# Optimization experiments

Measured on AMD Instinct MI355X. Metric: run time of the kernel, lower is better.

The kernel has to match this reference:

```python
import jax, jax.numpy as jnp
import numpy as np

D_MODEL = 512      # hidden_dim
D_INNER = 1024     # 2 * hidden_dim (Mamba expand=2)
D_STATE = 16       # SSM state size N
DT_RANK = 32       # hidden_dim // 16
NBLK = 4           # num_blocks
KCONV = 4          # depthwise conv kernel
NHEAD = 4
NUM_LANES = 6
LANE_DIM = 128


def _rms(x, w, eps=1e-5):
    return x * jax.lax.rsqrt(jnp.mean(x * x, axis=-1, keepdims=True) + eps) * w


def _selective_scan(u, delta, A, Bm, Cm, Dv):
    # u, delta: [B,L,d]; A: [d,N]; Bm, Cm: [B,L,N]; Dv: [d]
    dA = jnp.exp(delta[..., None] * A)                 # [B,L,d,N]
    dBu = (delta * u)[..., None] * Bm[:, :, None, :]   # [B,L,d,N]

    def step(h, xs):
        dA_t, dBu_t = xs
        h = dA_t * h + dBu_t
        return h, h

    h0 = jnp.zeros(dA.shape[:1] + dA.shape[2:], dA.dtype)  # [B,d,N]
    _, hs = jax.lax.scan(step, h0, (jnp.swapaxes(dA, 0, 1), jnp.swapaxes(dBu, 0, 1)))
    y = jnp.einsum('lbdn,bln->bld', hs, Cm)            # [B,L,d]
    return y + u * Dv


def _mamba(lane_features, lane_in_W, lane_in_b, norm_w, in_proj_W, conv_w, conv_b,
           x_proj_W, dt_proj_W, dt_proj_b, A_log, D_skip, out_proj_W, final_norm_w):
    x = lane_features @ lane_in_W + lane_in_b          # [B,L,D_MODEL]
    for i in range(NBLK):
        h = _rms(x, norm_w[i])
        xz = h @ in_proj_W[i]                          # [B,L,2*D_INNER]
        xc, z = jnp.split(xz, 2, axis=-1)
        xt = jnp.swapaxes(xc, 1, 2)                    # [B,d,L]
        conv = jax.lax.conv_general_dilated(
            xt, conv_w[i][:, None, :], (1,), [(KCONV - 1, 0)],
            feature_group_count=D_INNER,
            dimension_numbers=('NCH', 'OIH', 'NCH')) + conv_b[i][:, None]
        xc = jax.nn.silu(jnp.swapaxes(conv, 1, 2))     # causal depthwise conv + SiLU
        dbl = xc @ x_proj_W[i]
        dt = dbl[..., :DT_RANK]
        Bm = dbl[..., DT_RANK:DT_RANK + D_STATE]
        Cm = dbl[..., DT_RANK + D_STATE:]
        delta = jax.nn.softplus(dt @ dt_proj_W[i] + dt_proj_b[i])
        y = _selective_scan(xc, delta, -jnp.exp(A_log[i]), Bm, Cm, D_skip[i])
        x = x + (y * jax.nn.silu(z)) @ out_proj_W[i]
    return _rms(x, final_norm_w)


def _mha(q_in, kv_in, Wq, bq, Wk, bk, Wv, bv, Wo, bo):
    B, Lq, _ = q_in.shape
    Lk = kv_in.shape[1]
    dh = D_MODEL // NHEAD
    q = (q_in @ Wq + bq).reshape(B, Lq, NHEAD, dh).transpose(0, 2, 1, 3)
    k = (kv_in @ Wk + bk).reshape(B, Lk, NHEAD, dh).transpose(0, 2, 1, 3)
    v = (kv_in @ Wv + bv).reshape(B, Lk, NHEAD, dh).transpose(0, 2, 1, 3)
    attn = jax.nn.softmax(jnp.einsum('bhqd,bhkd->bhqk', q, k) / np.sqrt(dh).astype(np.float32), axis=-1)
    o = jnp.einsum('bhqk,bhkd->bhqd', attn, v).transpose(0, 2, 1, 3).reshape(B, Lq, D_MODEL)
    return o @ Wo + bo


def setup_inputs() -> dict:
    key = jax.random.key(0)
    ks = iter(jax.random.split(key, 40))
    def n(shape, s=0.02):
        return jax.random.normal(next(ks), shape, jnp.float32) * s
    inp = {}
    inp['agent_features'] = jax.random.normal(next(ks), (8, 256, D_MODEL), jnp.float32)
    inp['lane_features'] = jax.random.normal(next(ks), (8, 512, LANE_DIM), jnp.float32)
    inp['lane_in_W'] = n((LANE_DIM, D_MODEL))
    inp['lane_in_b'] = jnp.zeros((D_MODEL,), jnp.float32)
    inp['norm_w'] = jnp.ones((NBLK, D_MODEL), jnp.float32)
    inp['in_proj_W'] = n((NBLK, D_MODEL, 2 * D_INNER))
    inp['conv_w'] = n((NBLK, D_INNER, KCONV), 0.2)
    inp['conv_b'] = jnp.zeros((NBLK, D_INNER), jnp.float32)
    inp['x_proj_W'] = n((NBLK, D_INNER, DT_RANK + 2 * D_STATE))
    inp['dt_proj_W'] = n((NBLK, DT_RANK, D_INNER), 0.1)
    inp['dt_proj_b'] = n((NBLK, D_INNER), 0.1)
    inp['A_log'] = jnp.tile(jnp.log(jnp.arange(1, D_STATE + 1, dtype=jnp.float32)), (NBLK, D_INNER, 1))
    inp['D_skip'] = jnp.ones((NBLK, D_INNER), jnp.float32)
    inp['out_proj_W'] = n((NBLK, D_INNER, D_MODEL))
    inp['final_norm_w'] = jnp.ones((D_MODEL,), jnp.float32)
    for name in ['Wq', 'Wk', 'Wv', 'Wo']:
        inp[name] = n((D_MODEL, D_MODEL))
    for name in ['bq', 'bk', 'bv', 'bo']:
        inp[name] = jnp.zeros((D_MODEL,), jnp.float32)
    inp['lin_in_W'] = n((D_MODEL, D_MODEL))
    inp['lin_in_b'] = jnp.zeros((D_MODEL,), jnp.float32)
    inp['lin_out_W'] = n((D_MODEL, NUM_LANES))
    inp['lin_out_b'] = jnp.zeros((NUM_LANES,), jnp.float32)
    return inp


def reference(agent_features, lane_features, lane_in_W, lane_in_b, norm_w, in_proj_W,
              conv_w, conv_b, x_proj_W, dt_proj_W, dt_proj_b, A_log, D_skip, out_proj_W,
              final_norm_w, Wq, Wk, Wv, Wo, bq, bk, bv, bo,
              lin_in_W, lin_in_b, lin_out_W, lin_out_b):
    enhanced = _mamba(lane_features, lane_in_W, lane_in_b, norm_w, in_proj_W, conv_w,
                      conv_b, x_proj_W, dt_proj_W, dt_proj_b, A_log, D_skip,
                      out_proj_W, final_norm_w)
    attn_out = _mha(enhanced, agent_features, Wq, bq, Wk, bk, Wv, bv, Wo, bo)
    probs = (attn_out @ lin_in_W + lin_in_b) @ lin_out_W + lin_out_b
    preds = jnp.argmax(probs, axis=-1)
    return probs, preds
```

## Files before the change

### kernel.cpp

```cpp
#include <hip/hip_runtime.h>
#include <math.h>

#define BATCH 8
#define LSEQ 512
#define LAGENT 256
#define DMODEL 512
#define DINNER 1024
#define DSTATE 16
#define DTRANK 32
#define NHEAD 4
#define DHEAD 128
#define NLANES 6

typedef __attribute__((ext_vector_type(8))) short bf16x8;
typedef __attribute__((ext_vector_type(4))) float f32x4;

__device__ __forceinline__ void split3(float x, short& h, short& m, short& l)
{
    unsigned hb = __float_as_uint(x) & 0xFFFF0000u;
    h = (short)(hb >> 16);
    float r1 = x - __uint_as_float(hb);
    unsigned mb = __float_as_uint(r1) & 0xFFFF0000u;
    m = (short)(mb >> 16);
    float r2 = r1 - __uint_as_float(mb);
    l = (short)(__float_as_uint(r2) >> 16);
}

template<int BM, int BN, int WM, int WN>
__global__ __launch_bounds__(256)
void gemm6(const float* __restrict__ A, int lda,
           const float* __restrict__ W,
           const float* __restrict__ bias,
           float* __restrict__ C, int ldc,
           int M, int N, int K, int act, int addC)
{
    constexpr int MT = BM / WM / 16;
    constexpr int NT = BN / WN / 16;
    constexpr int ASL = BM / 16;
    constexpr int BSL = BN / 16;
    __shared__ short Asl[3][ASL * 520];
    __shared__ short Bsl[3][BSL * 520];

    const int tid = threadIdx.x;
    const int w = tid >> 6, lane = tid & 63;
    const int lrow = lane & 15, quad = lane >> 4;
    const int aslab0 = (w % WM) * MT;
    const int bslab0 = (w / WM) * NT;
    const int m0 = blockIdx.y * BM, n0 = blockIdx.x * BN;

    f32x4 acc[MT][NT] = {};

    for (int k0 = 0; k0 < K; k0 += 32) {
        __syncthreads();
#pragma unroll
        for (int i = 0; i < BM / 32; ++i) {
            int v = tid + 256 * i;
            int row = v >> 3;
            int kq = (v & 7) * 4;
            float4 val = *(const float4*)&A[(size_t)(m0 + row) * lda + k0 + kq];
            int off = (row >> 4) * 520 + (((kq >> 3) << 4) + (row & 15)) * 8 + (kq & 7);
            short h[4], mm_[4], l[4];
            split3(val.x, h[0], mm_[0], l[0]);
            split3(val.y, h[1], mm_[1], l[1]);
            split3(val.z, h[2], mm_[2], l[2]);
            split3(val.w, h[3], mm_[3], l[3]);
            *(short4*)&Asl[0][off] = make_short4(h[0], h[1], h[2], h[3]);
            *(short4*)&Asl[1][off] = make_short4(mm_[0], mm_[1], mm_[2], mm_[3]);
            *(short4*)&Asl[2][off] = make_short4(l[0], l[1], l[2], l[3]);
        }
        constexpr int NPQS = (BN == 128) ? 5 : 4;
#pragma unroll
        for (int i = 0; i < BN / 64; ++i) {
            int v = tid + 256 * i;
            int kp = v >> NPQS;
            int nc = (v & ((1 << NPQS) - 1)) * 4;
            int k1 = kp * 2;
            float4 r0 = *(const float4*)&W[(size_t)(k0 + k1) * N + n0 + nc];
            float4 r1 = *(const float4*)&W[(size_t)(k0 + k1 + 1) * N + n0 + nc];
            const float e0[4] = {r0.x, r0.y, r0.z, r0.w};
            const float e1[4] = {r1.x, r1.y, r1.z, r1.w};
#pragma unroll
            for (int e = 0; e < 4; ++e) {
                int n = nc + e;
                int off = (n >> 4) * 520 + (((k1 >> 3) << 4) + (n & 15)) * 8 + (k1 & 7);
                short h0, m0_, l0, h1, m1_, l1;
                split3(e0[e], h0, m0_, l0);
                split3(e1[e], h1, m1_, l1);
                *(short2*)&Bsl[0][off] = make_short2(h0, h1);
                *(short2*)&Bsl[1][off] = make_short2(m0_, m1_);
                *(short2*)&Bsl[2][off] = make_short2(l0, l1);
            }
        }
        __syncthreads();

        bf16x8 af[3][MT];
#pragma unroll
        for (int p = 0; p < 3; ++p)
#pragma unroll
            for (int i = 0; i < MT; ++i)
                af[p][i] = *(const bf16x8*)&Asl[p][(aslab0 + i) * 520 + lane * 8];

#pragma unroll
        for (int pb = 0; pb < 3; ++pb) {
            bf16x8 bfr[NT];
#pragma unroll
            for (int j = 0; j < NT; ++j)
                bfr[j] = *(const bf16x8*)&Bsl[pb][(bslab0 + j) * 520 + lane * 8];
            const int npa = (pb == 0) ? 3 : (pb == 1 ? 2 : 1);
#pragma unroll
            for (int pa = 0; pa < 3; ++pa) {
                if (pa >= npa) break;
#pragma unroll
                for (int i = 0; i < MT; ++i)
#pragma unroll
                    for (int j = 0; j < NT; ++j)
                        acc[i][j] = __builtin_amdgcn_mfma_f32_16x16x32_bf16(
                            af[pa][i], bfr[j], acc[i][j], 0, 0, 0);
            }
        }
    }

#pragma unroll
    for (int i = 0; i < MT; ++i) {
        int mbase = m0 + (aslab0 + i) * 16 + quad * 4;
#pragma unroll
        for (int j = 0; j < NT; ++j) {
            int n = n0 + (bslab0 + j) * 16 + lrow;
            float bv = bias ? bias[n] : 0.f;
#pragma unroll
            for (int r = 0; r < 4; ++r) {
                size_t off = (size_t)(mbase + r) * ldc + n;
                float v = acc[i][j][r] + bv;
                if (act == 1) v = (v > 20.f) ? v : log1pf(__expf(v));
                if (addC) v += C[off];
                C[off] = v;
            }
        }
    }
}

template<int BM, int BN, int WM, int WN>
__global__ __launch_bounds__(256)
void gemm6p(const unsigned short* __restrict__ Ap0,
            const unsigned short* __restrict__ Ap1,
            const unsigned short* __restrict__ Ap2, int lda,
            const float* __restrict__ W,
            const float* __restrict__ bias,
            float* __restrict__ C, int ldc,
            int M, int N, int K, int act, int addC)
{
    constexpr int MT = BM / WM / 16;
    constexpr int NT = BN / WN / 16;
    constexpr int ASL = BM / 16;
    constexpr int BSL = BN / 16;
    __shared__ short Asl[3][ASL * 520];
    __shared__ short Bsl[3][BSL * 520];

    const int tid = threadIdx.x;
    const int w = tid >> 6, lane = tid & 63;
    const int lrow = lane & 15, quad = lane >> 4;
    const int aslab0 = (w % WM) * MT;
    const int bslab0 = (w / WM) * NT;
    const int m0 = blockIdx.y * BM, n0 = blockIdx.x * BN;

    f32x4 acc[MT][NT] = {};

    for (int k0 = 0; k0 < K; k0 += 32) {
        __syncthreads();
#pragma unroll
        for (int i = 0; i < BM / 32; ++i) {
            int v = tid + 256 * i;
            int row = v >> 3;
            int kq = (v & 7) * 4;
            size_t g = (size_t)(m0 + row) * lda + k0 + kq;
            int off = (row >> 4) * 520 + (((kq >> 3) << 4) + (row & 15)) * 8 + (kq & 7);
            *(short4*)&Asl[0][off] = *(const short4*)&Ap0[g];
            *(short4*)&Asl[1][off] = *(const short4*)&Ap1[g];
            *(short4*)&Asl[2][off] = *(const short4*)&Ap2[g];
        }
        constexpr int NPQS = (BN == 128) ? 5 : 4;
#pragma unroll
        for (int i = 0; i < BN / 64; ++i) {
            int v = tid + 256 * i;
            int kp = v >> NPQS;
            int nc = (v & ((1 << NPQS) - 1)) * 4;
            int k1 = kp * 2;
            float4 r0 = *(const float4*)&W[(size_t)(k0 + k1) * N + n0 + nc];
            float4 r1 = *(const float4*)&W[(size_t)(k0 + k1 + 1) * N + n0 + nc];
            const float e0[4] = {r0.x, r0.y, r0.z, r0.w};
            const float e1[4] = {r1.x, r1.y, r1.z, r1.w};
#pragma unroll
            for (int e = 0; e < 4; ++e) {
                int n = nc + e;
                int off = (n >> 4) * 520 + (((k1 >> 3) << 4) + (n & 15)) * 8 + (k1 & 7);
                short h0, m0_, l0, h1, m1_, l1;
                split3(e0[e], h0, m0_, l0);
                split3(e1[e], h1, m1_, l1);
                *(short2*)&Bsl[0][off] = make_short2(h0, h1);
                *(short2*)&Bsl[1][off] = make_short2(m0_, m1_);
                *(short2*)&Bsl[2][off] = make_short2(l0, l1);
            }
        }
        __syncthreads();

        bf16x8 af[3][MT];
#pragma unroll
        for (int p = 0; p < 3; ++p)
#pragma unroll
            for (int i = 0; i < MT; ++i)
                af[p][i] = *(const bf16x8*)&Asl[p][(aslab0 + i) * 520 + lane * 8];

#pragma unroll
        for (int pb = 0; pb < 3; ++pb) {
            bf16x8 bfr[NT];
#pragma unroll
            for (int j = 0; j < NT; ++j)
                bfr[j] = *(const bf16x8*)&Bsl[pb][(bslab0 + j) * 520 + lane * 8];
            const int npa = (pb == 0) ? 3 : (pb == 1 ? 2 : 1);
#pragma unroll
            for (int pa = 0; pa < 3; ++pa) {
                if (pa >= npa) break;
#pragma unroll
                for (int i = 0; i < MT; ++i)
#pragma unroll
                    for (int j = 0; j < NT; ++j)
                        acc[i][j] = __builtin_amdgcn_mfma_f32_16x16x32_bf16(
                            af[pa][i], bfr[j], acc[i][j], 0, 0, 0);
            }
        }
    }

#pragma unroll
    for (int i = 0; i < MT; ++i) {
        int mbase = m0 + (aslab0 + i) * 16 + quad * 4;
#pragma unroll
        for (int j = 0; j < NT; ++j) {
            int n = n0 + (bslab0 + j) * 16 + lrow;
            float bv = bias ? bias[n] : 0.f;
#pragma unroll
            for (int r = 0; r < 4; ++r) {
                size_t off = (size_t)(mbase + r) * ldc + n;
                float v = acc[i][j][r] + bv;
                if (act == 1) v = (v > 20.f) ? v : log1pf(__expf(v));
                if (addC) v += C[off];
                C[off] = v;
            }
        }
    }
}

__global__ __launch_bounds__(256)
void gemm6sk(const float* __restrict__ A, int lda,
             const float* __restrict__ W, int N,
             float* __restrict__ P, int M, int KC)
{
    constexpr int BM = 64, BN = 64, WM = 2, WN = 2;
    constexpr int MT = BM / WM / 16, NT = BN / WN / 16;
    __shared__ short Asl[3][4 * 520];
    __shared__ short Bsl[3][4 * 520];

    const int tid = threadIdx.x;
    const int w = tid >> 6, lane = tid & 63;
    const int lrow = lane & 15, quad = lane >> 4;
    const int aslab0 = (w % WM) * MT;
    const int bslab0 = (w / WM) * NT;
    const int m0 = blockIdx.y * BM, n0 = blockIdx.x * BN;
    const int kbeg = blockIdx.z * KC;

    f32x4 acc[MT][NT] = {};

    for (int k0 = kbeg; k0 < kbeg + KC; k0 += 32) {
        __syncthreads();
#pragma unroll
        for (int i = 0; i < BM / 32; ++i) {
            int v = tid + 256 * i;
            int row = v >> 3;
            int kq = (v & 7) * 4;
            float4 val = *(const float4*)&A[(size_t)(m0 + row) * lda + k0 + kq];
            int off = (row >> 4) * 520 + (((kq >> 3) << 4) + (row & 15)) * 8 + (kq & 7);
            short h[4], mm_[4], l[4];
            split3(val.x, h[0], mm_[0], l[0]);
            split3(val.y, h[1], mm_[1], l[1]);
            split3(val.z, h[2], mm_[2], l[2]);
            split3(val.w, h[3], mm_[3], l[3]);
            *(short4*)&Asl[0][off] = make_short4(h[0], h[1], h[2], h[3]);
            *(short4*)&Asl[1][off] = make_short4(mm_[0], mm_[1], mm_[2], mm_[3]);
            *(short4*)&Asl[2][off] = make_short4(l[0], l[1], l[2], l[3]);
        }
        {
            int v = tid;
            int kp = v >> 4;
            int nc = (v & 15) * 4;
            int k1 = kp * 2;
            float4 r0 = *(const float4*)&W[(size_t)(k0 + k1) * N + n0 + nc];
            float4 r1 = *(const float4*)&W[(size_t)(k0 + k1 + 1) * N + n0 + nc];
            const float e0[4] = {r0.x, r0.y, r0.z, r0.w};
            const float e1[4] = {r1.x, r1.y, r1.z, r1.w};
#pragma unroll
            for (int e = 0; e < 4; ++e) {
                int n = nc + e;
                int off = (n >> 4) * 520 + (((k1 >> 3) << 4) + (n & 15)) * 8 + (k1 & 7);
                short h0, m0_, l0, h1, m1_, l1;
                split3(e0[e], h0, m0_, l0);
                split3(e1[e], h1, m1_, l1);
                *(short2*)&Bsl[0][off] = make_short2(h0, h1);
                *(short2*)&Bsl[1][off] = make_short2(m0_, m1_);
                *(short2*)&Bsl[2][off] = make_short2(l0, l1);
            }
        }
        __syncthreads();

        bf16x8 af[3][MT];
#pragma unroll
        for (int p = 0; p < 3; ++p)
#pragma unroll
            for (int i = 0; i < MT; ++i)
                af[p][i] = *(const bf16x8*)&Asl[p][(aslab0 + i) * 520 + lane * 8];

#pragma unroll
        for (int pb = 0; pb < 3; ++pb) {
            bf16x8 bfr[NT];
#pragma unroll
            for (int j = 0; j < NT; ++j)
                bfr[j] = *(const bf16x8*)&Bsl[pb][(bslab0 + j) * 520 + lane * 8];
            const int npa = (pb == 0) ? 3 : (pb == 1 ? 2 : 1);
#pragma unroll
            for (int pa = 0; pa < 3; ++pa) {
                if (pa >= npa) break;
#pragma unroll
                for (int i = 0; i < MT; ++i)
#pragma unroll
                    for (int j = 0; j < NT; ++j)
                        acc[i][j] = __builtin_amdgcn_mfma_f32_16x16x32_bf16(
                            af[pa][i], bfr[j], acc[i][j], 0, 0, 0);
            }
        }
    }

    float* Pz = P + (size_t)blockIdx.z * M * N;
#pragma unroll
    for (int i = 0; i < MT; ++i) {
        int mbase = m0 + (aslab0 + i) * 16 + quad * 4;
#pragma unroll
        for (int j = 0; j < NT; ++j) {
            int n = n0 + (bslab0 + j) * 16 + lrow;
#pragma unroll
            for (int r = 0; r < 4; ++r)
                Pz[(size_t)(mbase + r) * N + n] = acc[i][j][r];
        }
    }
}

__global__ __launch_bounds__(256)
void xred_k(const float* __restrict__ P, float* __restrict__ D)
{
    int i = blockIdx.x * 256 + threadIdx.x;
    const float4* p = (const float4*)P;
    float4 a = p[i];
#pragma unroll
    for (int z = 1; z < 8; ++z) {
        float4 b = p[(size_t)z * 65536 + i];
        a.x += b.x; a.y += b.y; a.z += b.z; a.w += b.w;
    }
    ((float4*)D)[i] = a;
}

__global__ __launch_bounds__(256)
void rmsnorm3_k(const float* __restrict__ X, const float* __restrict__ w,
                unsigned short* __restrict__ P0, unsigned short* __restrict__ P1,
                unsigned short* __restrict__ P2)
{
    int wid = threadIdx.x >> 6, lane = threadIdx.x & 63;
    int row = blockIdx.x * 4 + wid;
    const float* xr = X + (size_t)row * DMODEL;
    float v[8];
    float ss = 0.f;
#pragma unroll
    for (int j = 0; j < 8; ++j) { v[j] = xr[lane + 64 * j]; ss = fmaf(v[j], v[j], ss); }
#pragma unroll
    for (int off = 32; off >= 1; off >>= 1) ss += __shfl_xor(ss, off);
    float scale = rsqrtf(ss * (1.f / 512.f) + 1e-5f);
#pragma unroll
    for (int j = 0; j < 8; ++j) {
        int col = lane + 64 * j;
        float val = v[j] * scale * w[col];
        short hh, mm, ll;
        split3(val, hh, mm, ll);
        size_t o = (size_t)row * DMODEL + col;
        P0[o] = (unsigned short)hh;
        P1[o] = (unsigned short)mm;
        P2[o] = (unsigned short)ll;
    }
}

__global__ __launch_bounds__(256)
void conv_silu_k(const float* __restrict__ XZ, const float* __restrict__ cw,
                 const float* __restrict__ cb, float* __restrict__ XC)
{
    int idx = blockIdx.x * 256 + threadIdx.x;
    int d4 = (idx & 255) * 4;
    int t = (idx >> 8) & 511;
    int b = idx >> 17;
    float4 wv[4];
#pragma unroll
    for (int e = 0; e < 4; ++e) wv[e] = *(const float4*)&cw[(d4 + e) * 4];
    float4 bv = *(const float4*)&cb[d4];
    float s[4] = {bv.x, bv.y, bv.z, bv.w};
#pragma unroll
    for (int k = 0; k < 4; ++k) {
        int tt = t + k - 3;
        if (tt >= 0) {
            float4 x = *(const float4*)&XZ[((size_t)(b * 512 + tt)) * 2048 + d4];
            const float xe[4] = {x.x, x.y, x.z, x.w};
            const float we[4] = {wv[0][k], wv[1][k], wv[2][k], wv[3][k]};
#pragma unroll
            for (int e = 0; e < 4; ++e) s[e] = fmaf(we[e], xe[e], s[e]);
        }
    }
    float4 o;
    o.x = s[0] / (1.f + __expf(-s[0]));
    o.y = s[1] / (1.f + __expf(-s[1]));
    o.z = s[2] / (1.f + __expf(-s[2]));
    o.w = s[3] / (1.f + __expf(-s[3]));
    *(float4*)&XC[((size_t)(b * 512 + t)) * 1024 + d4] = o;
}

__global__ __launch_bounds__(128)
void scan1_k(const float* __restrict__ DELTA, const float* __restrict__ XC,
             const float* __restrict__ DBL, const float* __restrict__ A_log,
             const float* __restrict__ Dsk, float* __restrict__ Y,
             float* __restrict__ SC, float* __restrict__ DS)
{
    __shared__ float BC[64][32];
    const int tid = threadIdx.x;
    const int d = blockIdx.x * 128 + tid;
    const int chunk = blockIdx.y;
    const int b = blockIdx.z;
    const int t0 = chunk * 64;

#pragma unroll
    for (int i = 0; i < 16; ++i) {
        int idx = tid + 128 * i;
        int t = idx >> 5, j = idx & 31;
        BC[t][j] = DBL[(size_t)(b * 512 + t0 + t) * 64 + 32 + j];
    }
    float Ac[16];
#pragma unroll
    for (int n = 0; n < 16; ++n) Ac[n] = -__expf(A_log[d * 16 + n]);
    float Dv = Dsk[d];
    __syncthreads();

    const float* dp = DELTA + ((size_t)(b * 512 + t0)) * 1024 + d;
    const float* up = XC    + ((size_t)(b * 512 + t0)) * 1024 + d;
    float* yp       = Y     + ((size_t)(b * 512 + t0)) * 1024 + d;

    float h[16];
#pragma unroll
    for (int n = 0; n < 16; ++n) h[n] = 0.f;
    float dsum = 0.f;

#pragma unroll 2
    for (int t = 0; t < 64; ++t) {
        float delta = dp[t * 1024];
        float u = up[t * 1024];
        dsum += delta;
        float du = delta * u;
        float y = 0.f;
#pragma unroll
        for (int n = 0; n < 16; ++n) {
            h[n] = fmaf(__expf(delta * Ac[n]), h[n], du * BC[t][n]);
            y = fmaf(h[n], BC[t][16 + n], y);
        }
        yp[t * 1024] = fmaf(u, Dv, y);
    }

    float* sc = SC + ((size_t)((b * 8 + chunk) * 1024 + d)) * 16;
#pragma unroll
    for (int n = 0; n < 16; ++n) sc[n] = h[n];
    DS[(size_t)(b * 8 + chunk) * 1024 + d] = dsum;
}

__global__ __launch_bounds__(256)
void scan2_k(const float* __restrict__ A_log, float* __restrict__ SC,
             const float* __restrict__ DS)
{
    int gid = blockIdx.x * 256 + threadIdx.x;
    int n = gid & 15;
    int d = (gid >> 4) & 1023;
    int b = gid >> 14;
    float Ac = -__expf(A_log[d * 16 + n]);
    float carry = 0.f;
#pragma unroll
    for (int c = 0; c < 8; ++c) {
        size_t off = ((size_t)((b * 8 + c) * 1024 + d)) * 16 + n;
        float s = SC[off];
        SC[off] = carry;
        carry = fmaf(__expf(Ac * DS[(size_t)(b * 8 + c) * 1024 + d]), carry, s);
    }
}

__global__ __launch_bounds__(128)
void scan3_k(const float* __restrict__ DELTA, const float* __restrict__ DBL,
             const float* __restrict__ A_log, const float* __restrict__ H0,
             const float* __restrict__ XZ, float* __restrict__ Y)
{
    __shared__ float Cs[64][16];
    const int tid = threadIdx.x;
    const int d = blockIdx.x * 128 + tid;
    const int chunk = blockIdx.y;
    const int b = blockIdx.z;
    const int t0 = chunk * 64;

#pragma unroll
    for (int i = 0; i < 8; ++i) {
        int idx = tid + 128 * i;
        int t = idx >> 4, j = idx & 15;
        Cs[t][j] = DBL[(size_t)(b * 512 + t0 + t) * 64 + 48 + j];
    }
    float Ac[16], h0[16];
#pragma unroll
    for (int n = 0; n < 16; ++n) Ac[n] = -__expf(A_log[d * 16 + n]);
    const float* h0p = H0 + ((size_t)((b * 8 + chunk) * 1024 + d)) * 16;
#pragma unroll
    for (int n = 0; n < 16; ++n) h0[n] = h0p[n];
    __syncthreads();

    const float* dp = DELTA + ((size_t)(b * 512 + t0)) * 1024 + d;
    const float* zp = XZ    + ((size_t)(b * 512 + t0)) * 2048 + 1024 + d;
    float* yp       = Y     + ((size_t)(b * 512 + t0)) * 1024 + d;

    float cum = 0.f;
    if (chunk == 0) {
#pragma unroll 2
        for (int t = 0; t < 64; ++t) {
            float z = zp[t * 2048];
            yp[t * 1024] *= z / (1.f + __expf(-z));
        }
    } else {
#pragma unroll 2
        for (int t = 0; t < 64; ++t) {
            float delta = dp[t * 1024];
            cum += delta;
            float p = 0.f;
#pragma unroll
            for (int n = 0; n < 16; ++n)
                p = fmaf(h0[n] * __expf(Ac[n] * cum), Cs[t][n], p);
            float z = zp[t * 2048];
            float yv = yp[t * 1024] + p;
            yp[t * 1024] = yv * (z / (1.f + __expf(-z)));
        }
    }
}

__global__ __launch_bounds__(256, 1)
void attn_mfma(const float* __restrict__ Qm, const float* __restrict__ Km,
               const float* __restrict__ Vm, float* __restrict__ CTX)
{
    __shared__ short KVs[3][16 * 520];
    __shared__ float Ps[4][16 * 260];
    const int tid = threadIdx.x;
    const int w = tid >> 6, lane = tid & 63;
    const int lrow = lane & 15, quad = lane >> 4;
    const int b = blockIdx.z, h = blockIdx.y;
    const int qw = blockIdx.x * 64 + w * 16;

    bf16x8 qf[3][4];
    {
        const float* qp = Qm + ((size_t)(b * 512 + qw + lrow)) * 512 + h * 128 + quad * 8;
#pragma unroll
        for (int kb = 0; kb < 4; ++kb) {
            float4 v0 = *(const float4*)(qp + kb * 32);
            float4 v1 = *(const float4*)(qp + kb * 32 + 4);
            const float e[8] = {v0.x, v0.y, v0.z, v0.w, v1.x, v1.y, v1.z, v1.w};
#pragma unroll
            for (int j = 0; j < 8; ++j) {
                short hh, mm, ll;
                split3(e[j], hh, mm, ll);
                qf[0][kb][j] = hh; qf[1][kb][j] = mm; qf[2][kb][j] = ll;
            }
        }
    }

    const int sdd = (tid & 31) * 4;
    const int skvb = tid >> 5;
    f32x4 sa[4][4] = {};

    float4 kpre[8];
#pragma unroll
    for (int i = 0; i < 8; ++i)
        kpre[i] = *(const float4*)&Km[((size_t)(b * 256 + skvb + 8 * i)) * 512 + h * 128 + sdd];

    for (int c = 0; c < 4; ++c) {
        if (c) __syncthreads();
        {
            const int kb = sdd >> 5, qd = (sdd >> 3) & 3, jd = sdd & 7;
#pragma unroll
            for (int i = 0; i < 8; ++i) {
                int kv = skvb + 8 * i;
                int off = ((kv >> 4) * 4 + kb) * 520 + ((kv & 15) + 16 * qd) * 8 + jd;
                short h0,m0,l0,h1,m1,l1,h2,m2,l2,h3,m3,l3;
                split3(kpre[i].x,h0,m0,l0); split3(kpre[i].y,h1,m1,l1);
                split3(kpre[i].z,h2,m2,l2); split3(kpre[i].w,h3,m3,l3);
                *(short4*)&KVs[0][off] = make_short4(h0,h1,h2,h3);
                *(short4*)&KVs[1][off] = make_short4(m0,m1,m2,m3);
                *(short4*)&KVs[2][off] = make_short4(l0,l1,l2,l3);
            }
        }
        if (c < 3) {
#pragma unroll
            for (int i = 0; i < 8; ++i)
                kpre[i] = *(const float4*)&Km[((size_t)(b * 256 + (c + 1) * 64 + skvb + 8 * i)) * 512 + h * 128 + sdd];
        }
        __syncthreads();
#pragma unroll
        for (int s = 0; s < 4; ++s) {
#pragma unroll
            for (int kb = 0; kb < 4; ++kb) {
                bf16x8 kf[3];
#pragma unroll
                for (int p = 0; p < 3; ++p)
                    kf[p] = *(const bf16x8*)&KVs[p][(s * 4 + kb) * 520 + lane * 8];
                sa[c][s] = __builtin_amdgcn_mfma_f32_16x16x32_bf16(qf[0][kb], kf[0], sa[c][s], 0, 0, 0);
                sa[c][s] = __builtin_amdgcn_mfma_f32_16x16x32_bf16(qf[0][kb], kf[1], sa[c][s], 0, 0, 0);
                sa[c][s] = __builtin_amdgcn_mfma_f32_16x16x32_bf16(qf[1][kb], kf[0], sa[c][s], 0, 0, 0);
                sa[c][s] = __builtin_amdgcn_mfma_f32_16x16x32_bf16(qf[0][kb], kf[2], sa[c][s], 0, 0, 0);
                sa[c][s] = __builtin_amdgcn_mfma_f32_16x16x32_bf16(qf[1][kb], kf[1], sa[c][s], 0, 0, 0);
                sa[c][s] = __builtin_amdgcn_mfma_f32_16x16x32_bf16(qf[2][kb], kf[0], sa[c][s], 0, 0, 0);
            }
        }
    }

    const float scale = 0.08838834764831845f;
    float mx[4] = {-1e30f, -1e30f, -1e30f, -1e30f};
#pragma unroll
    for (int c = 0; c < 4; ++c)
#pragma unroll
        for (int s = 0; s < 4; ++s)
#pragma unroll
            for (int r = 0; r < 4; ++r) {
                sa[c][s][r] *= scale;
                mx[r] = fmaxf(mx[r], sa[c][s][r]);
            }
#pragma unroll
    for (int r = 0; r < 4; ++r) {
        mx[r] = fmaxf(mx[r], __shfl_xor(mx[r], 1));
        mx[r] = fmaxf(mx[r], __shfl_xor(mx[r], 2));
        mx[r] = fmaxf(mx[r], __shfl_xor(mx[r], 4));
        mx[r] = fmaxf(mx[r], __shfl_xor(mx[r], 8));
    }
    float sum[4] = {0.f, 0.f, 0.f, 0.f};
#pragma unroll
    for (int c = 0; c < 4; ++c)
#pragma unroll
        for (int s = 0; s < 4; ++s)
#pragma unroll
            for (int r = 0; r < 4; ++r) {
                float e = __expf(sa[c][s][r] - mx[r]);
                sa[c][s][r] = e;
                sum[r] += e;
            }
#pragma unroll
    for (int r = 0; r < 4; ++r) {
        sum[r] += __shfl_xor(sum[r], 1);
        sum[r] += __shfl_xor(sum[r], 2);
        sum[r] += __shfl_xor(sum[r], 4);
        sum[r] += __shfl_xor(sum[r], 8);
        sum[r] = 1.f / sum[r];
    }
    {
        float* ps = &Ps[w][0];
#pragma unroll
        for (int c = 0; c < 4; ++c)
#pragma unroll
            for (int s = 0; s < 4; ++s)
#pragma unroll
                for (int r = 0; r < 4; ++r)
                    ps[(quad * 4 + r) * 260 + c * 64 + s * 16 + lrow] = sa[c][s][r] * sum[r];
    }

    const int vdd4 = (tid & 31) * 4;
    const int vkvg = tid >> 5;
    f32x4 oa[8] = {};
    float4 vpre[8];
#pragma unroll
    for (int i = 0; i < 2; ++i) {
        int kv0 = (vkvg + 8 * i) * 4;
#pragma unroll
        for (int rr = 0; rr < 4; ++rr)
            vpre[i * 4 + rr] = *(const float4*)&Vm[((size_t)(b * 256 + kv0 + rr)) * 512 + h * 128 + vdd4];
    }

    for (int c = 0; c < 4; ++c) {
        __syncthreads();
        {
#pragma unroll
            for (int i = 0; i < 2; ++i) {
                int kv0 = (vkvg + 8 * i) * 4;
                int kb2 = kv0 >> 5, qk = (kv0 >> 3) & 3, jb = kv0 & 7;
                const float4 r0 = vpre[i * 4 + 0], r1 = vpre[i * 4 + 1];
                const float4 r2 = vpre[i * 4 + 2], r3 = vpre[i * 4 + 3];
                const float ve[4][4] = {{r0.x, r1.x, r2.x, r3.x},
                                        {r0.y, r1.y, r2.y, r3.y},
                                        {r0.z, r1.z, r2.z, r3.z},
                                        {r0.w, r1.w, r2.w, r3.w}};
#pragma unroll
                for (int e = 0; e < 4; ++e) {
                    int dd = vdd4 + e;
                    int off = ((dd >> 4) * 2 + kb2) * 520 + ((dd & 15) + 16 * qk) * 8 + jb;
                    short h0,m0,l0,h1,m1,l1,h2,m2,l2,h3,m3,l3;
                    split3(ve[e][0],h0,m0,l0); split3(ve[e][1],h1,m1,l1);
                    split3(ve[e][2],h2,m2,l2); split3(ve[e][3],h3,m3,l3);
                    *(short4*)&KVs[0][off] = make_short4(h0,h1,h2,h3);
                    *(short4*)&KVs[1][off] = make_short4(m0,m1,m2,m3);
                    *(short4*)&KVs[2][off] = make_short4(l0,l1,l2,l3);
                }
            }
        }
        if (c < 3) {
#pragma unroll
            for (int i = 0; i < 2; ++i) {
                int kv0 = (vkvg + 8 * i) * 4;
#pragma unroll
                for (int rr = 0; rr < 4; ++rr)
                    vpre[i * 4 + rr] = *(const float4*)&Vm[((size_t)(b * 256 + (c + 1) * 64 + kv0 + rr)) * 512 + h * 128 + vdd4];
            }
        }
        __syncthreads();
#pragma unroll
        for (int kb2 = 0; kb2 < 2; ++kb2) {
            const float* pp = &Ps[w][lrow * 260 + c * 64 + kb2 * 32 + quad * 8];
            float4 a0 = *(const float4*)pp;
            float4 a1 = *(const float4*)(pp + 4);
            const float e[8] = {a0.x, a0.y, a0.z, a0.w, a1.x, a1.y, a1.z, a1.w};
            bf16x8 af[3];
#pragma unroll
            for (int j = 0; j < 8; ++j) {
                short hh, mm, ll;
                split3(e[j], hh, mm, ll);
                af[0][j] = hh; af[1][j] = mm; af[2][j] = ll;
            }
#pragma unroll
            for (int s = 0; s < 8; ++s) {
                bf16x8 vf[3];
#pragma unroll
                for (int p = 0; p < 3; ++p)
                    vf[p] = *(const bf16x8*)&KVs[p][(s * 2 + kb2) * 520 + lane * 8];
                oa[s] = __builtin_amdgcn_mfma_f32_16x16x32_bf16(af[0], vf[0], oa[s], 0, 0, 0);
                oa[s] = __builtin_amdgcn_mfma_f32_16x16x32_bf16(af[0], vf[1], oa[s], 0, 0, 0);
                oa[s] = __builtin_amdgcn_mfma_f32_16x16x32_bf16(af[1], vf[0], oa[s], 0, 0, 0);
                oa[s] = __builtin_amdgcn_mfma_f32_16x16x32_bf16(af[0], vf[2], oa[s], 0, 0, 0);
                oa[s] = __builtin_amdgcn_mfma_f32_16x16x32_bf16(af[1], vf[1], oa[s], 0, 0, 0);
                oa[s] = __builtin_amdgcn_mfma_f32_16x16x32_bf16(af[2], vf[0], oa[s], 0, 0, 0);
            }
        }
    }

#pragma unroll
    for (int s = 0; s < 8; ++s)
#pragma unroll
        for (int r = 0; r < 4; ++r)
            CTX[((size_t)(b * 512 + qw + quad * 4 + r)) * 512 + h * 128 + s * 16 + lrow] = oa[s][r];
}

__global__ __launch_bounds__(256)
void head_k(const float* __restrict__ T2, const float* __restrict__ Wout,
            const float* __restrict__ bout, float* __restrict__ out)
{
    int wid = threadIdx.x >> 6, lane = threadIdx.x & 63;
    int row = blockIdx.x * 4 + wid;
    float acc[6] = {0.f, 0.f, 0.f, 0.f, 0.f, 0.f};
    const float* tr = T2 + (size_t)row * 512;
#pragma unroll
    for (int j = 0; j < 8; ++j) {
        int k = lane + 64 * j;
        float t = tr[k];
#pragma unroll
        for (int c = 0; c < 6; ++c) acc[c] = fmaf(t, Wout[k * 6 + c], acc[c]);
    }
#pragma unroll
    for (int c = 0; c < 6; ++c) {
#pragma unroll
        for (int off = 32; off >= 1; off >>= 1) acc[c] += __shfl_xor(acc[c], off);
    }
    if (lane == 0) {
        float best = -1e30f;
        int bi = 0;
#pragma unroll
        for (int c = 0; c < 6; ++c) {
            float v = acc[c] + bout[c];
            out[(size_t)row * 6 + c] = v;
            if (v > best) { best = v; bi = c; }
        }
        out[(size_t)4096 * 6 + row] = (float)bi;
    }
}

extern "C" void kernel_launch(void* const* d_in, const int* in_sizes, int n_in,
                              void* d_out, int out_size, void* d_ws, size_t ws_size,
                              hipStream_t stream)
{
    (void)in_sizes; (void)n_in; (void)out_size; (void)ws_size;
    const float* agent      = (const float*)d_in[0];
    const float* lane       = (const float*)d_in[1];
    const float* lane_in_W  = (const float*)d_in[2];
    const float* lane_in_b  = (const float*)d_in[3];
    const float* norm_w     = (const float*)d_in[4];
    const float* in_proj_W  = (const float*)d_in[5];
    const float* conv_w     = (const float*)d_in[6];
    const float* conv_b     = (const float*)d_in[7];
    const float* x_proj_W   = (const float*)d_in[8];
    const float* dt_proj_W  = (const float*)d_in[9];
    const float* dt_proj_b  = (const float*)d_in[10];
    const float* A_log      = (const float*)d_in[11];
    const float* D_skip     = (const float*)d_in[12];
    const float* out_proj_W = (const float*)d_in[13];
    const float* final_norm_w = (const float*)d_in[14];
    const float* Wq = (const float*)d_in[15];
    const float* Wk = (const float*)d_in[16];
    const float* Wv = (const float*)d_in[17];
    const float* Wo = (const float*)d_in[18];
    const float* bq = (const float*)d_in[19];
    const float* bk = (const float*)d_in[20];
    const float* bv = (const float*)d_in[21];
    const float* bo = (const float*)d_in[22];
    const float* lin_in_W  = (const float*)d_in[23];
    const float* lin_in_b  = (const float*)d_in[24];
    const float* lin_out_W = (const float*)d_in[25];
    const float* lin_out_b = (const float*)d_in[26];

    float* ws = (float*)d_ws;
    float* X     = ws;
    float* H     = X + (1 << 21);
    float* XZ    = H + (1 << 21);
    float* XC    = XZ + (1 << 23);
    float* DELTA = XC + (1 << 22);
    float* Y     = DELTA + (1 << 22);
    float* DBL   = Y + (1 << 22);
    unsigned short* Hp0 = (unsigned short*)H;
    unsigned short* Hp1 = (unsigned short*)(H + (1 << 20));
    unsigned short* Hp2 = (unsigned short*)Y;
    float* PART  = Y + (1 << 20);
    float* SCb   = H;
    float* DSb   = H + (1 << 20);
    float* Qb  = XZ;
    float* Kb  = XZ + (1 << 21);
    float* Vb  = Kb + (1 << 20);
    float* CTX = Vb + (1 << 20);
    float* AO  = CTX + (1 << 21);
    float* T2  = XC;

    dim3 blk(256);
    dim3 sblk(128);
    dim3 sgrid(8, 8, 8);

    gemm6<128, 64, 2, 2><<<dim3(8, 32), blk, 0, stream>>>(
        lane, 128, lane_in_W, lane_in_b, X, 512, 4096, 512, 128, 0, 0);

    for (int i = 0; i < 4; ++i) {
        rmsnorm3_k<<<1024, blk, 0, stream>>>(X, norm_w + i * 512, Hp0, Hp1, Hp2);
        gemm6p<128, 128, 2, 2><<<dim3(16, 32), blk, 0, stream>>>(
            Hp0, Hp1, Hp2, 512, in_proj_W + (size_t)i * 512 * 2048, nullptr, XZ, 2048,
            4096, 2048, 512, 0, 0);
        conv_silu_k<<<4096, blk, 0, stream>>>(XZ, conv_w + i * 4096, conv_b + i * 1024, XC);
        gemm6sk<<<dim3(1, 64, 8), blk, 0, stream>>>(
            XC, 1024, x_proj_W + (size_t)i * 1024 * 64, 64, PART, 4096, 128);
        xred_k<<<256, blk, 0, stream>>>(PART, DBL);
        gemm6<128, 64, 2, 2><<<dim3(16, 32), blk, 0, stream>>>(
            DBL, 64, dt_proj_W + (size_t)i * 32 * 1024, dt_proj_b + i * 1024,
            DELTA, 1024, 4096, 1024, 32, 1, 0);
        scan1_k<<<sgrid, sblk, 0, stream>>>(DELTA, XC, DBL, A_log + (size_t)i * 1024 * 16,
                                            D_skip + i * 1024, Y, SCb, DSb);
        scan2_k<<<512, blk, 0, stream>>>(A_log + (size_t)i * 1024 * 16, SCb, DSb);
        scan3_k<<<sgrid, sblk, 0, stream>>>(DELTA, DBL, A_log + (size_t)i * 1024 * 16,
                                            SCb, XZ, Y);
        gemm6<128, 64, 2, 2><<<dim3(8, 32), blk, 0, stream>>>(
            Y, 1024, out_proj_W + (size_t)i * 1024 * 512, nullptr, X, 512,
            4096, 512, 1024, 0, 1);
    }

    rmsnorm3_k<<<1024, blk, 0, stream>>>(X, final_norm_w, Hp0, Hp1, Hp2);

    gemm6p<128, 64, 2, 2><<<dim3(8, 32), blk, 0, stream>>>(
        Hp0, Hp1, Hp2, 512, Wq, bq, Qb, 512, 4096, 512, 512, 0, 0);
    gemm6<64, 64, 2, 2><<<dim3(8, 32), blk, 0, stream>>>(
        agent, 512, Wk, bk, Kb, 512, 2048, 512, 512, 0, 0);
    gemm6<64, 64, 2, 2><<<dim3(8, 32), blk, 0, stream>>>(
        agent, 512, Wv, bv, Vb, 512, 2048, 512, 512, 0, 0);
    attn_mfma<<<dim3(8, 4, 8), blk, 0, stream>>>(Qb, Kb, Vb, CTX);
    gemm6<128, 64, 2, 2><<<dim3(8, 32), blk, 0, stream>>>(
        CTX, 512, Wo, bo, AO, 512, 4096, 512, 512, 0, 0);
    gemm6<128, 64, 2, 2><<<dim3(8, 32), blk, 0, stream>>>(
        AO, 512, lin_in_W, lin_in_b, T2, 512, 4096, 512, 512, 0, 0);
    head_k<<<1024, blk, 0, stream>>>(T2, lin_out_W, lin_out_b, (float*)d_out);
}
```

Before: 1.367 ms.

## Pre-split weights into bf16x3 fragment-ordered planes before GEMMs

Adds a wsplit_k kernel that converts each fp32 weight matrix into three bf16 planes (hi/mid/lo) already laid out in MFMA fragment order. The GEMM kernels then copy B tiles straight into shared memory with int4 loads, with no per-tile split3 arithmetic or scattered short2 stores. Some GEMMs also move to 64x64 tiles with twice as many blocks. The cost is extra weight-split launches on every call, plus workspace buffers reused across stages (WPL aliases XC, T2 moves to DELTA).

```diff
diff --git a/kernel.cpp b/kernel.cpp
--- a/kernel.cpp
+++ b/kernel.cpp
@@ -24,6 +24,30 @@
     m = (short)(mb >> 16);
     float r2 = r1 - __uint_as_float(mb);
     l = (short)(__float_as_uint(r2) >> 16);
+}
+
+__global__ __launch_bounds__(256)
+void wsplit_k(const float* __restrict__ W, short* __restrict__ Wp, int K, int N)
+{
+    int gid = blockIdx.x * 256 + threadIdx.x;
+    int lane = gid & 63;
+    int rest = gid >> 6;
+    int nsl = N >> 4;
+    int ns = rest % nsl, kc = rest / nsl;
+    int lrow = lane & 15, quad = lane >> 4;
+    const float* src = W + (size_t)(kc * 32 + quad * 8) * N + ns * 16 + lrow;
+    bf16x8 h, m, l;
+#pragma unroll
+    for (int j = 0; j < 8; ++j) {
+        short hh, mm, ll;
+        split3(src[(size_t)j * N], hh, mm, ll);
+        h[j] = hh; m[j] = mm; l[j] = ll;
+    }
+    size_t planeS = (size_t)K * N;
+    size_t base = ((size_t)(kc * nsl + ns)) * 512 + lane * 8;
+    *(bf16x8*)&Wp[base] = h;
+    *(bf16x8*)&Wp[planeS + base] = m;
+    *(bf16x8*)&Wp[2 * planeS + base] = l;
 }
 
 template<int BM, int BN, int WM, int WN>
@@ -141,10 +165,10 @@
 
 template<int BM, int BN, int WM, int WN>
 __global__ __launch_bounds__(256)
-void gemm6p(const unsigned short* __restrict__ Ap0,
+void gemm6f(const unsigned short* __restrict__ Ap0,
             const unsigned short* __restrict__ Ap1,
             const unsigned short* __restrict__ Ap2, int lda,
-            const float* __restrict__ W,
+            const short* __restrict__ Wp,
             const float* __restrict__ bias,
             float* __restrict__ C, int ldc,
             int M, int N, int K, int act, int addC)
@@ -153,8 +177,10 @@
     constexpr int NT = BN / WN / 16;
     constexpr int ASL = BM / 16;
     constexpr int BSL = BN / 16;
+    constexpr int BITER = (3 * BSL) / 4;
+    constexpr int PSH = (BSL == 8) ? 9 : 8;
     __shared__ short Asl[3][ASL * 520];
-    __shared__ short Bsl[3][BSL * 520];
+    __shared__ short Bsl[3][BSL * 512];
 
     const int tid = threadIdx.x;
     const int w = tid >> 6, lane = tid & 63;
@@ -162,6 +188,7 @@
     const int aslab0 = (w % WM) * MT;
     const int bslab0 = (w / WM) * NT;
     const int m0 = blockIdx.y * BM, n0 = blockIdx.x * BN;
+    const size_t planeS = (size_t)K * N;
 
     f32x4 acc[MT][NT] = {};
 
@@ -178,27 +205,14 @@
             *(short4*)&Asl[1][off] = *(const short4*)&Ap1[g];
             *(short4*)&Asl[2][off] = *(const short4*)&Ap2[g];
         }
-        constexpr int NPQS = (BN == 128) ? 5 : 4;
-#pragma unroll
-        for (int i = 0; i < BN / 64; ++i) {
-            int v = tid + 256 * i;
-            int kp = v >> NPQS;
-            int nc = (v & ((1 << NPQS) - 1)) * 4;
-            int k1 = kp * 2;
-            float4 r0 = *(const float4*)&W[(size_t)(k0 + k1) * N + n0 + nc];
-            float4 r1 = *(const float4*)&W[(size_t)(k0 + k1 + 1) * N + n0 + nc];
-            const float e0[4] = {r0.x, r0.y, r0.z, r0.w};
-            const float e1[4] = {r1.x, r1.y, r1.z, r1.w};
-#pragma unroll
-            for (int e = 0; e < 4; ++e) {
-                int n = nc + e;
-                int off = (n >> 4) * 520 + (((k1 >> 3) << 4) + (n & 15)) * 8 + (k1 & 7);
-                short h0, m0_, l0, h1, m1_, l1;
-                split3(e0[e], h0, m0_, l0);
-                split3(e1[e], h1, m1_, l1);
-                *(short2*)&Bsl[0][off] = make_short2(h0, h1);
-                *(short2*)&Bsl[1][off] = make_short2(m0_, m1_);
-                *(short2*)&Bsl[2][off] = make_short2(l0, l1);
+        {
+            const short* wb = Wp + ((size_t)(k0 >> 5) * (N >> 4) + (n0 >> 4)) * 512;
+#pragma unroll
+            for (int i = 0; i < BITER; ++i) {
+                int idx = tid + 256 * i;
+                int p = idx >> PSH;
+                int r = idx & ((1 << PSH) - 1);
+                *(int4*)&Bsl[p][r * 8] = *(const int4*)(wb + p * planeS + r * 8);
             }
         }
         __syncthreads();
@@ -215,7 +229,7 @@
             bf16x8 bfr[NT];
 #pragma unroll
             for (int j = 0; j < NT; ++j)
-                bfr[j] = *(const bf16x8*)&Bsl[pb][(bslab0 + j) * 520 + lane * 8];
+                bfr[j] = *(const bf16x8*)&Bsl[pb][(bslab0 + j) * 512 + lane * 8];
             const int npa = (pb == 0) ? 3 : (pb == 1 ? 2 : 1);
 #pragma unroll
             for (int pa = 0; pa < 3; ++pa) {
@@ -249,15 +263,22 @@
     }
 }
 
+template<int BM, int BN, int WM, int WN>
 __global__ __launch_bounds__(256)
-void gemm6sk(const float* __restrict__ A, int lda,
-             const float* __restrict__ W, int N,
-             float* __restrict__ P, int M, int KC)
-{
-    constexpr int BM = 64, BN = 64, WM = 2, WN = 2;
-    constexpr int MT = BM / WM / 16, NT = BN / WN / 16;
-    __shared__ short Asl[3][4 * 520];
-    __shared__ short Bsl[3][4 * 520];
+void gemm6g(const float* __restrict__ A, int lda,
+            const short* __restrict__ Wp,
+            const float* __restrict__ bias,
+            float* __restrict__ C, int ldc,
+            int M, int N, int K, int act, int addC)
+{
+    constexpr int MT = BM / WM / 16;
+    constexpr int NT = BN / WN / 16;
+    constexpr int ASL = BM / 16;
+    constexpr int BSL = BN / 16;
+    constexpr int BITER = (3 * BSL) / 4;
+    constexpr int PSH = (BSL == 8) ? 9 : 8;
+    __shared__ short Asl[3][ASL * 520];
+    __shared__ short Bsl[3][BSL * 512];
 
     const int tid = threadIdx.x;
     const int w = tid >> 6, lane = tid & 63;
@@ -265,11 +286,11 @@
     const int aslab0 = (w % WM) * MT;
     const int bslab0 = (w / WM) * NT;
     const int m0 = blockIdx.y * BM, n0 = blockIdx.x * BN;
-    const int kbeg = blockIdx.z * KC;
+    const size_t planeS = (size_t)K * N;
 
     f32x4 acc[MT][NT] = {};
 
-    for (int k0 = kbeg; k0 < kbeg + KC; k0 += 32) {
+    for (int k0 = 0; k0 < K; k0 += 32) {
         __syncthreads();
 #pragma unroll
         for (int i = 0; i < BM / 32; ++i) {
@@ -288,6 +309,102 @@
             *(short4*)&Asl[2][off] = make_short4(l[0], l[1], l[2], l[3]);
         }
         {
+            const short* wb = Wp + ((size_t)(k0 >> 5) * (N >> 4) + (n0 >> 4)) * 512;
+#pragma unroll
+            for (int i = 0; i < BITER; ++i) {
+                int idx = tid + 256 * i;
+                int p = idx >> PSH;
+                int r = idx & ((1 << PSH) - 1);
+                *(int4*)&Bsl[p][r * 8] = *(const int4*)(wb + p * planeS + r * 8);
+            }
+        }
+        __syncthreads();
+
+        bf16x8 af[3][MT];
+#pragma unroll
+        for (int p = 0; p < 3; ++p)
+#pragma unroll
+            for (int i = 0; i < MT; ++i)
+                af[p][i] = *(const bf16x8*)&Asl[p][(aslab0 + i) * 520 + lane * 8];
+
+#pragma unroll
+        for (int pb = 0; pb < 3; ++pb) {
+            bf16x8 bfr[NT];
+#pragma unroll
+            for (int j = 0; j < NT; ++j)
+                bfr[j] = *(const bf16x8*)&Bsl[pb][(bslab0 + j) * 512 + lane * 8];
+            const int npa = (pb == 0) ? 3 : (pb == 1 ? 2 : 1);
+#pragma unroll
+            for (int pa = 0; pa < 3; ++pa) {
+                if (pa >= npa) break;
+#pragma unroll
+                for (int i = 0; i < MT; ++i)
+#pragma unroll
+                    for (int j = 0; j < NT; ++j)
+                        acc[i][j] = __builtin_amdgcn_mfma_f32_16x16x32_bf16(
+                            af[pa][i], bfr[j], acc[i][j], 0, 0, 0);
+            }
+        }
+    }
+
+#pragma unroll
+    for (int i = 0; i < MT; ++i) {
+        int mbase = m0 + (aslab0 + i) * 16 + quad * 4;
+#pragma unroll
+        for (int j = 0; j < NT; ++j) {
+            int n = n0 + (bslab0 + j) * 16 + lrow;
+            float bv = bias ? bias[n] : 0.f;
+#pragma unroll
+            for (int r = 0; r < 4; ++r) {
+                size_t off = (size_t)(mbase + r) * ldc + n;
+                float v = acc[i][j][r] + bv;
+                if (act == 1) v = (v > 20.f) ? v : log1pf(__expf(v));
+                if (addC) v += C[off];
+                C[off] = v;
+            }
+        }
+    }
+}
+
+__global__ __launch_bounds__(256)
+void gemm6sk(const float* __restrict__ A, int lda,
+             const float* __restrict__ W, int N,
+             float* __restrict__ P, int M, int KC)
+{
+    constexpr int BM = 64, BN = 64, WM = 2, WN = 2;
+    constexpr int MT = BM / WM / 16, NT = BN / WN / 16;
+    __shared__ short Asl[3][4 * 520];
+    __shared__ short Bsl[3][4 * 520];
+
+    const int tid = threadIdx.x;
+    const int w = tid >> 6, lane = tid & 63;
+    const int lrow = lane & 15, quad = lane >> 4;
+    const int aslab0 = (w % WM) * MT;
+    const int bslab0 = (w / WM) * NT;
+    const int m0 = blockIdx.y * BM, n0 = blockIdx.x * BN;
+    const int kbeg = blockIdx.z * KC;
+
+    f32x4 acc[MT][NT] = {};
+
+    for (int k0 = kbeg; k0 < kbeg + KC; k0 += 32) {
+        __syncthreads();
+#pragma unroll
+        for (int i = 0; i < BM / 32; ++i) {
+            int v = tid + 256 * i;
+            int row = v >> 3;
+            int kq = (v & 7) * 4;
+            float4 val = *(const float4*)&A[(size_t)(m0 + row) * lda + k0 + kq];
+            int off = (row >> 4) * 520 + (((kq >> 3) << 4) + (row & 15)) * 8 + (kq & 7);
+            short h[4], mm_[4], l[4];
+            split3(val.x, h[0], mm_[0], l[0]);
+            split3(val.y, h[1], mm_[1], l[1]);
+            split3(val.z, h[2], mm_[2], l[2]);
+            split3(val.w, h[3], mm_[3], l[3]);
+            *(short4*)&Asl[0][off] = make_short4(h[0], h[1], h[2], h[3]);
+            *(short4*)&Asl[1][off] = make_short4(mm_[0], mm_[1], mm_[2], mm_[3]);
+            *(short4*)&Asl[2][off] = make_short4(l[0], l[1], l[2], l[3]);
+        }
+        {
             int v = tid;
             int kp = v >> 4;
             int nc = (v & 15) * 4;
@@ -337,7 +454,7 @@
         }
     }
 
-    float* Pz = P + (size_t)blockIdx.z * M * N;
+    float* Pz = P + (size_t)blockIdx.z * M * 64;
 #pragma unroll
     for (int i = 0; i < MT; ++i) {
         int mbase = m0 + (aslab0 + i) * 16 + quad * 4;
@@ -346,7 +463,7 @@
             int n = n0 + (bslab0 + j) * 16 + lrow;
 #pragma unroll
             for (int r = 0; r < 4; ++r)
-                Pz[(size_t)(mbase + r) * N + n] = acc[i][j][r];
+                Pz[(size_t)(mbase + r) * 64 + n] = acc[i][j][r];
         }
     }
 }
@@ -842,25 +959,27 @@
     float* PART  = Y + (1 << 20);
     float* SCb   = H;
     float* DSb   = H + (1 << 20);
+    short* WPL   = (short*)XC;
     float* Qb  = XZ;
     float* Kb  = XZ + (1 << 21);
     float* Vb  = Kb + (1 << 20);
     float* CTX = Vb + (1 << 20);
     float* AO  = CTX + (1 << 21);
-    float* T2  = XC;
+    float* T2  = DELTA;
 
     dim3 blk(256);
     dim3 sblk(128);
     dim3 sgrid(8, 8, 8);
 
-    gemm6<128, 64, 2, 2><<<dim3(8, 32), blk, 0, stream>>>(
-        lane, 128, lane_in_W, lane_in_b, X, 512, 4096, 512, 128, 0, 0);
+    wsplit_k<<<32, blk, 0, stream>>>(lane_in_W, WPL, 128, 512);
+    gemm6g<128, 64, 2, 2><<<dim3(8, 32), blk, 0, stream>>>(
+        lane, 128, WPL, lane_in_b, X, 512, 4096, 512, 128, 0, 0);
 
     for (int i = 0; i < 4; ++i) {
         rmsnorm3_k<<<1024, blk, 0, stream>>>(X, norm_w + i * 512, Hp0, Hp1, Hp2);
-        gemm6p<128, 128, 2, 2><<<dim3(16, 32), blk, 0, stream>>>(
-            Hp0, Hp1, Hp2, 512, in_proj_W + (size_t)i * 512 * 2048, nullptr, XZ, 2048,
-            4096, 2048, 512, 0, 0);
+        wsplit_k<<<512, blk, 0, stream>>>(in_proj_W + (size_t)i * 512 * 2048, WPL, 512, 2048);
+        gemm6f<128, 128, 2, 2><<<dim3(16, 32), blk, 0, stream>>>(
+            Hp0, Hp1, Hp2, 512, WPL, nullptr, XZ, 2048, 4096, 2048, 512, 0, 0);
         conv_silu_k<<<4096, blk, 0, stream>>>(XZ, conv_w + i * 4096, conv_b + i * 1024, XC);
         gemm6sk<<<dim3(1, 64, 8), blk, 0, stream>>>(
             XC, 1024, x_proj_W + (size_t)i * 1024 * 64, 64, PART, 4096, 128);
@@ -871,25 +990,36 @@
         scan1_k<<<sgrid, sblk, 0, stream>>>(DELTA, XC, DBL, A_log + (size_t)i * 1024 * 16,
                                             D_skip + i * 1024, Y, SCb, DSb);
         scan2_k<<<512, blk, 0, stream>>>(A_log + (size_t)i * 1024 * 16, SCb, DSb);
+        wsplit_k<<<256, blk, 0, stream>>>(out_proj_W + (size_t)i * 1024 * 512, WPL, 1024, 512);
         scan3_k<<<sgrid, sblk, 0, stream>>>(DELTA, DBL, A_log + (size_t)i * 1024 * 16,
                                             SCb, XZ, Y);
-        gemm6<128, 64, 2, 2><<<dim3(8, 32), blk, 0, stream>>>(
-            Y, 1024, out_proj_W + (size_t)i * 1024 * 512, nullptr, X, 512,
-            4096, 512, 1024, 0, 1);
+        gemm6g<64, 64, 2, 2><<<dim3(8, 64), blk, 0, stream>>>(
+            Y, 1024, WPL, nullptr, X, 512, 4096, 512, 1024, 0, 1);
     }
 
     rmsnorm3_k<<<1024, blk, 0, stream>>>(X, final_norm_w, Hp0, Hp1, Hp2);
 
-    gemm6p<128, 64, 2, 2><<<dim3(8, 32), blk, 0, stream>>>(
-        Hp0, Hp1, Hp2, 512, Wq, bq, Qb, 512, 4096, 512, 512, 0, 0);
-    gemm6<64, 64, 2, 2><<<dim3(8, 32), blk, 0, stream>>>(
-        agent, 512, Wk, bk, Kb, 512, 2048, 512, 512, 0, 0);
-    gemm6<64, 64, 2, 2><<<dim3(8, 32), blk, 0, stream>>>(
-        agent, 512, Wv, bv, Vb, 512, 2048, 512, 512, 0, 0);
+    short* WPq = WPL;
+    short* WPk = WPL + 786432;
+    short* WPv = WPL + 2 * 786432;
+    short* WPo = WPL + 3 * 786432;
+    short* WPn = WPL + 4 * 786432;
+    wsplit_k<<<128, blk, 0, stream>>>(Wq, WPq, 512, 512);
+    wsplit_k<<<128, blk, 0, stream>>>(Wk, WPk, 512, 512);
+    wsplit_k<<<128, blk, 0, stream>>>(Wv, WPv, 512, 512);
+    wsplit_k<<<128, blk, 0, stream>>>(Wo, WPo, 512, 512);
+    wsplit_k<<<128, blk, 0, stream>>>(lin_in_W, WPn, 512, 512);
+
+    gemm6f<128, 64, 2, 2><<<dim3(8, 32), blk, 0, stream>>>(
+        Hp0, Hp1, Hp2, 512, WPq, bq, Qb, 512, 4096, 512, 512, 0, 0);
+    gemm6g<64, 64, 2, 2><<<dim3(8, 32), blk, 0, stream>>>(
+        agent, 512, WPk, bk, Kb, 512, 2048, 512, 512, 0, 0);
+    gemm6g<64, 64, 2, 2><<<dim3(8, 32), blk, 0, stream>>>(
+        agent, 512, WPv, bv, Vb, 512, 2048, 512, 512, 0, 0);
     attn_mfma<<<dim3(8, 4, 8), blk, 0, stream>>>(Qb, Kb, Vb, CTX);
-    gemm6<128, 64, 2, 2><<<dim3(8, 32), blk, 0, stream>>>(
-        CTX, 512, Wo, bo, AO, 512, 4096, 512, 512, 0, 0);
-    gemm6<128, 64, 2, 2><<<dim3(8, 32), blk, 0, stream>>>(
-        AO, 512, lin_in_W, lin_in_b, T2, 512, 4096, 512, 512, 0, 0);
+    gemm6g<64, 64, 2, 2><<<dim3(8, 64), blk, 0, stream>>>(
+        CTX, 512, WPo, bo, AO, 512, 4096, 512, 512, 0, 0);
+    gemm6g<64, 64, 2, 2><<<dim3(8, 64), blk, 0, stream>>>(
+        AO, 512, WPn, lin_in_b, T2, 512, 4096, 512, 512, 0, 0);
     head_k<<<1024, blk, 0, stream>>>(T2, lin_out_W, lin_out_b, (float*)d_out);
 }
```

New measurement: 1.297 ms. 1.05x faster.
